# Kernel optimization log

Measured on AMD Instinct MI355X. Metric: run time of the kernel, lower is better.

Reference implementation:

```python
import jax, jax.numpy as jnp
import numpy as np

START_IDX = 1
STOP_IDX = 2
VOCAB = 32000
EMB = 512
HID = 512


def setup_inputs() -> dict:
    key = jax.random.key(0)
    ks = jax.random.split(key, 10)
    B, T = 64, 50
    x = jax.random.normal(ks[0], (B, HID), dtype=jnp.float32)
    labels = jax.random.randint(ks[1], (B, T), 0, VOCAB, dtype=jnp.int64)
    s = 0.02
    emb = jax.random.normal(ks[2], (VOCAB, EMB), dtype=jnp.float32) * s
    W_ih = jax.random.normal(ks[3], (4 * HID, EMB), dtype=jnp.float32) * s
    W_hh = jax.random.normal(ks[4], (4 * HID, HID), dtype=jnp.float32) * s
    b_ih = jax.random.normal(ks[5], (4 * HID,), dtype=jnp.float32) * s
    b_hh = jax.random.normal(ks[6], (4 * HID,), dtype=jnp.float32) * s
    fc_W = jax.random.normal(ks[7], (VOCAB, HID), dtype=jnp.float32) * s
    fc_b = jax.random.normal(ks[8], (VOCAB,), dtype=jnp.float32) * s
    return {"x": x, "labels": labels, "emb": emb, "W_ih": W_ih, "W_hh": W_hh,
            "b_ih": b_ih, "b_hh": b_hh, "fc_W": fc_W, "fc_b": fc_b}


def _decode_loss(x, labels, emb, W_ih, W_hh, b_ih, b_hh, fc_W, fc_b):
    B, T = labels.shape
    # teacher-forced inputs: [START, y_0..y_{T-1}]; targets: [y_0..y_{T-1}, STOP]
    inputs = jnp.concatenate([jnp.full((B, 1), START_IDX, labels.dtype), labels], axis=1)
    targets = jnp.concatenate([labels, jnp.full((B, 1), STOP_IDX, labels.dtype)], axis=1)
    x_emb = emb[inputs]                       # [B, T+1, E]
    x_emb_t = jnp.swapaxes(x_emb, 0, 1)       # [T+1, B, E]

    def step(carry, xt):
        h, c = carry
        gates = xt @ W_ih.T + b_ih + h @ W_hh.T + b_hh   # [B, 4H]
        i, f, g, o = jnp.split(gates, 4, axis=-1)         # torch gate order i,f,g,o
        i = jax.nn.sigmoid(i); f = jax.nn.sigmoid(f)
        g = jnp.tanh(g); o = jax.nn.sigmoid(o)
        c = f * c + i * g
        h = o * jnp.tanh(c)
        return (h, c), h

    # init_states(x[i]): hidden and cell initialized from image feature
    (_, _), hs = jax.lax.scan(step, (x, x), x_emb_t)      # hs: [T+1, B, H]
    logits = hs @ fc_W.T + fc_b                            # [T+1, B, V]
    logp = jax.nn.log_softmax(logits, axis=-1)
    tgt = jnp.swapaxes(targets, 0, 1)[..., None]           # [T+1, B, 1]
    nll = -jnp.take_along_axis(logp, tgt, axis=-1)         # [T+1, B, 1]
    # original: per-step CrossEntropyLoss on batch of 1, summed over steps, / batch_size
    return nll.sum() / B


def reference(x, labels, emb, W_ih, W_hh, b_ih, b_hh, fc_W, fc_b):
    return _decode_loss(x, labels, emb, W_ih, W_hh, b_ih, b_hh, fc_W, fc_b)
```

## Files before the change

kernel.cpp:

```cpp
#include <hip/hip_runtime.h>
#include <cstddef>
#include <cstdint>

#define B_  64
#define T_  51
#define H_  512
#define G4_ 2048
#define V_  32000
#define R_  (T_ * B_)
#define NHF (T_ * 128)

typedef __attribute__((ext_vector_type(8))) short bf16x8;
typedef __attribute__((ext_vector_type(4))) float f32x4;
typedef __attribute__((ext_vector_type(4))) unsigned int u32x4;
typedef unsigned long long ull;

__device__ __forceinline__ uint16_t f2bf(float f) {
    uint32_t u = __float_as_uint(f);
    u += 0x7FFFu + ((u >> 16) & 1u);
    return (uint16_t)(u >> 16);
}
__device__ __forceinline__ float bf2f(uint32_t h) { return __uint_as_float(h << 16); }

__device__ __forceinline__ void ldsc(u32x4& d, const uint32_t* p) {
    asm volatile("global_load_dwordx4 %0, %1, off sc0 sc1" : "=v"(d) : "v"(p));
}
__device__ __forceinline__ void ldq2(ull& d, const uint16_t* p) {
    asm volatile("global_load_dwordx2 %0, %1, off sc0 sc1" : "=v"(d) : "v"(p));
}
__device__ __forceinline__ uint32_t ldflag(const uint32_t* p) {
    uint32_t v;
    asm volatile("global_load_dword %0, %1, off sc0 sc1\n\ts_waitcnt vmcnt(0)"
                 : "=v"(v) : "v"(p));
    return v;
}
__device__ __forceinline__ void stflag(uint32_t* p, uint32_t v) {
    asm volatile("global_store_dword %0, %1, off sc0 sc1" :: "v"(p), "v"(v) : "memory");
}
__device__ __forceinline__ void stsh(uint16_t* p, uint32_t v) {
    asm volatile("global_store_short %0, %1, off sc0 sc1" :: "v"(p), "v"(v) : "memory");
}
__device__ __forceinline__ void stq(uint16_t* p, ull v) {
    asm volatile("global_store_dwordx2 %0, %1, off sc0 sc1" :: "v"(p), "v"(v) : "memory");
}

__device__ __forceinline__ void gl_lds16(const void* g, void* l) {
    __builtin_amdgcn_global_load_lds((const __attribute__((address_space(1))) void*)g,
                                     (__attribute__((address_space(3))) void*)l, 16, 0, 0);
}

__global__ __launch_bounds__(256) void k0_init(float* __restrict__ sumexp,
                                               uint32_t* __restrict__ flags) {
    int i = blockIdx.x * 256 + threadIdx.x;
    if (i < R_) sumexp[i] = 0.f;
    if (i < NHF + 512) flags[i] = 0;
}

template<int DOFC>
__global__ __launch_bounds__(256) void k12p(const float* __restrict__ x,
                                            const int* __restrict__ labels,
                                            const float* __restrict__ emb,
                                            const float* __restrict__ W_ih,
                                            const float* __restrict__ b_ih,
                                            const float* __restrict__ b_hh,
                                            const float* __restrict__ W_hh,
                                            const float* __restrict__ fc_W,
                                            uint16_t* __restrict__ fcwb,
                                            uint16_t* __restrict__ XgT,
                                            uint16_t* __restrict__ hs,
                                            uint32_t* __restrict__ flags) {
    __shared__ uint16_t smem[64 * 520];
    const int bid  = blockIdx.x;
    const int tid  = threadIdx.x;
    const int w    = tid >> 6;
    const int lane = tid & 63;
    const int l15  = lane & 15;
    const int lhi  = lane >> 4;

    if (bid >= 32) {
        uint16_t* Al = smem;
        uint16_t* Bl = smem + 64 * 72;
        for (int id = bid - 32; id < 408; id += 224) {
            const int t  = id >> 3;
            const int n0 = (id & 7) * 256;
            f32x4 acc[4][4];
            #pragma unroll
            for (int mi = 0; mi < 4; ++mi)
                #pragma unroll
                for (int nf = 0; nf < 4; ++nf) acc[mi][nf] = (f32x4){0.f, 0.f, 0.f, 0.f};
            for (int k0 = 0; k0 < H_; k0 += 64) {
                #pragma unroll
                for (int r = 0; r < 2; ++r) {
                    int idx = r * 256 + tid, row = idx >> 3, seg = idx & 7;
                    int tok = (t == 0) ? 1 : labels[row * 50 + (t - 1)];
                    const float* s = emb + (size_t)tok * H_ + k0 + seg * 8;
                    float4 f0 = *(const float4*)s;
                    float4 f1 = *(const float4*)(s + 4);
                    union { uint16_t h[8]; uint4 u; } p;
                    p.h[0]=f2bf(f0.x); p.h[1]=f2bf(f0.y); p.h[2]=f2bf(f0.z); p.h[3]=f2bf(f0.w);
                    p.h[4]=f2bf(f1.x); p.h[5]=f2bf(f1.y); p.h[6]=f2bf(f1.z); p.h[7]=f2bf(f1.w);
                    *(uint4*)(Al + row * 72 + seg * 8) = p.u;
                }
                #pragma unroll
                for (int r = 0; r < 8; ++r) {
                    int idx = r * 256 + tid, row = idx >> 3, seg = idx & 7;
                    const float* s = W_ih + (size_t)(n0 + row) * H_ + k0 + seg * 8;
                    float4 f0 = *(const float4*)s;
                    float4 f1 = *(const float4*)(s + 4);
                    union { uint16_t h[8]; uint4 u; } p;
                    p.h[0]=f2bf(f0.x); p.h[1]=f2bf(f0.y); p.h[2]=f2bf(f0.z); p.h[3]=f2bf(f0.w);
                    p.h[4]=f2bf(f1.x); p.h[5]=f2bf(f1.y); p.h[6]=f2bf(f1.z); p.h[7]=f2bf(f1.w);
                    *(uint4*)(Bl + row * 72 + seg * 8) = p.u;
                }
                __syncthreads();
                #pragma unroll
                for (int ks = 0; ks < 2; ++ks) {
                    bf16x8 a[4];
                    #pragma unroll
                    for (int mi = 0; mi < 4; ++mi)
                        a[mi] = *(const bf16x8*)(Al + (mi * 16 + l15) * 72 + ks * 32 + lhi * 8);
                    #pragma unroll
                    for (int nf = 0; nf < 4; ++nf) {
                        bf16x8 b = *(const bf16x8*)(Bl + (w * 64 + nf * 16 + l15) * 72 + ks * 32 + lhi * 8);
                        #pragma unroll
                        for (int mi = 0; mi < 4; ++mi)
                            acc[mi][nf] = __builtin_amdgcn_mfma_f32_16x16x32_bf16(a[mi], b, acc[mi][nf], 0, 0, 0);
                    }
                }
                __syncthreads();
            }
            float bias[4];
            #pragma unroll
            for (int nf = 0; nf < 4; ++nf) {
                int col = n0 + w * 64 + nf * 16 + l15;
                bias[nf] = b_ih[col] + b_hh[col];
            }
            #pragma unroll
            for (int mi = 0; mi < 4; ++mi)
                #pragma unroll
                for (int nf = 0; nf < 4; ++nf) {
                    const int col = n0 + w * 64 + nf * 16 + l15;
                    const int g = col >> 9, u = col & 511;
                    const int b = mi * 16 + lhi * 4;
                    union { uint16_t h[4]; ull q; } pk;
                    #pragma unroll
                    for (int q = 0; q < 4; ++q) pk.h[q] = f2bf(acc[mi][nf][q] + bias[nf]);
                    stq(XgT + ((size_t)(t * 512 + u) * 4 + g) * 64 + b, pk.q);
                }
            asm volatile("s_waitcnt vmcnt(0)" ::: "memory");
            __syncthreads();
            if (tid == 0) stflag(flags + NHF + t * 8 + (n0 >> 8), 1u);
        }
        if (DOFC) {
            const int n8 = (V_ * H_) / 8;
            for (int i = (bid - 32) * 256 + tid; i < n8; i += 224 * 256) {
                const float4* s = (const float4*)fc_W + (size_t)i * 2;
                float4 f0 = s[0], f1 = s[1];
                union { uint16_t h[8]; uint4 u; } p;
                p.h[0]=f2bf(f0.x); p.h[1]=f2bf(f0.y); p.h[2]=f2bf(f0.z); p.h[3]=f2bf(f0.w);
                p.h[4]=f2bf(f1.x); p.h[5]=f2bf(f1.y); p.h[6]=f2bf(f1.z); p.h[7]=f2bf(f1.w);
                ((uint4*)fcwb)[i] = p.u;
            }
        }
        return;
    }

    uint16_t* Wl = smem;
    const int u0   = bid * 16;
    const int arow = w * 16 + l15;
    {
        const int c = tid >> 2;
        const int q = tid & 3;
        const int j = (c >> 4) * 512 + u0 + (c & 15);
        const float* src = W_hh + (size_t)j * H_ + q * 128;
        uint16_t* dst = Wl + c * 520 + q * 128;
        #pragma unroll
        for (int i = 0; i < 128; i += 8) {
            float4 f0 = *(const float4*)(src + i);
            float4 f1 = *(const float4*)(src + i + 4);
            union { uint16_t h[8]; uint4 u; } p;
            p.h[0]=f2bf(f0.x); p.h[1]=f2bf(f0.y); p.h[2]=f2bf(f0.z); p.h[3]=f2bf(f0.w);
            p.h[4]=f2bf(f1.x); p.h[5]=f2bf(f1.y); p.h[6]=f2bf(f1.z); p.h[7]=f2bf(f1.w);
            *(uint4*)(dst + i) = p.u;
        }
    }
    float cst[4];
    #pragma unroll
    for (int q = 0; q < 4; ++q)
        cst[q] = x[(size_t)(w * 16 + lhi * 4 + q) * H_ + u0 + l15];
    __syncthreads();

    for (int t = 0; t < T_; ++t) {
        const uint32_t* fp = flags;
        bool dopoll = false;
        if (t > 0 && lane < 32)      { fp = flags + (size_t)(t - 1) * 128 + lane * 4 + w; dopoll = true; }
        else if (lane >= 32 && lane < 40) { fp = flags + NHF + t * 8 + (lane - 32); dopoll = true; }
        else if (t == 0 && lane < 8) { fp = flags + NHF + (lane); dopoll = true; }
        for (;;) {
            uint32_t fv = 1;
            if (dopoll) fv = ldflag(fp);
            if (!__any((int)(fv == 0))) break;
            __builtin_amdgcn_s_sleep(1);
        }
        __builtin_amdgcn_sched_barrier(0);

        u32x4 ha[16];
        ull xgp[4];
        if (t == 0) {
            const float* xb = x + (size_t)arow * H_ + lhi * 8;
            #pragma unroll
            for (int ks = 0; ks < 16; ++ks) {
                float4 f0 = *(const float4*)(xb + ks * 32);
                float4 f1 = *(const float4*)(xb + ks * 32 + 4);
                union { uint16_t h[8]; u32x4 u; } p;
                p.h[0]=f2bf(f0.x); p.h[1]=f2bf(f0.y); p.h[2]=f2bf(f0.z); p.h[3]=f2bf(f0.w);
                p.h[4]=f2bf(f1.x); p.h[5]=f2bf(f1.y); p.h[6]=f2bf(f1.z); p.h[7]=f2bf(f1.w);
                ha[ks] = p.u;
            }
        } else {
            const uint16_t* hb = hs + ((size_t)(t - 1) * 64 + arow) * H_ + lhi * 8;
            #pragma unroll
            for (int ks = 0; ks < 16; ++ks)
                ldsc(ha[ks], (const uint32_t*)(hb + ks * 32));
        }
        #pragma unroll
        for (int g = 0; g < 4; ++g)
            ldq2(xgp[g], XgT + ((size_t)(t * 512 + u0 + l15) * 4 + g) * 64 + w * 16 + lhi * 4);

        f32x4 acc[4];
        #pragma unroll
        for (int nf = 0; nf < 4; ++nf) acc[nf] = (f32x4){0.f, 0.f, 0.f, 0.f};
        if (t != 0) { asm volatile("s_waitcnt vmcnt(12)" ::: "memory");
                      __builtin_amdgcn_sched_barrier(0); }
        #pragma unroll
        for (int ks = 0; ks < 8; ++ks) {
            union { u32x4 u; bf16x8 v; } au; au.u = ha[ks];
            #pragma unroll
            for (int nf = 0; nf < 4; ++nf) {
                bf16x8 b = *(const bf16x8*)(Wl + (nf * 16 + l15) * 520 + ks * 32 + lhi * 8);
                acc[nf] = __builtin_amdgcn_mfma_f32_16x16x32_bf16(au.v, b, acc[nf], 0, 0, 0);
            }
        }
        asm volatile("s_waitcnt vmcnt(0)" ::: "memory");
        __builtin_amdgcn_sched_barrier(0);
        #pragma unroll
        for (int ks = 8; ks < 16; ++ks) {
            union { u32x4 u; bf16x8 v; } au; au.u = ha[ks];
            #pragma unroll
            for (int nf = 0; nf < 4; ++nf) {
                bf16x8 b = *(const bf16x8*)(Wl + (nf * 16 + l15) * 520 + ks * 32 + lhi * 8);
                acc[nf] = __builtin_amdgcn_mfma_f32_16x16x32_bf16(au.v, b, acc[nf], 0, 0, 0);
            }
        }
        #pragma unroll
        for (int q = 0; q < 4; ++q) {
            const int b = w * 16 + lhi * 4 + q;
            float gi = acc[0][q] + bf2f((uint32_t)((xgp[0] >> (16 * q)) & 0xFFFF));
            float gf = acc[1][q] + bf2f((uint32_t)((xgp[1] >> (16 * q)) & 0xFFFF));
            float gg = acc[2][q] + bf2f((uint32_t)((xgp[2] >> (16 * q)) & 0xFFFF));
            float go = acc[3][q] + bf2f((uint32_t)((xgp[3] >> (16 * q)) & 0xFFFF));
            float si = 1.f / (1.f + __expf(-gi));
            float sf = 1.f / (1.f + __expf(-gf));
            float tg = tanhf(gg);
            float so = 1.f / (1.f + __expf(-go));
            float cc = sf * cst[q] + si * tg;
            cst[q] = cc;
            stsh(hs + (size_t)(t * 64 + b) * H_ + u0 + l15, (uint32_t)f2bf(so * tanhf(cc)));
        }
        asm volatile("s_waitcnt vmcnt(0)" ::: "memory");
        if (lane == 0) stflag(flags + (size_t)t * 128 + bid * 4 + w, (uint32_t)(t + 1));
    }
}

template<int CVT>
__global__ __launch_bounds__(512, 4) void k3_mfma(const uint16_t* __restrict__ hsb,
                                                  const void* __restrict__ fcw,
                                                  const float* __restrict__ fc_b,
                                                  const int* __restrict__ labels,
                                                  float* __restrict__ sumexp,
                                                  float* __restrict__ tgtlog) {
    __shared__ uint16_t Al[128 * 64];
    __shared__ uint16_t Bl[256 * 64];
    const int flat = blockIdx.x;
    const int xcd  = flat & 7;
    const int slot = flat >> 3;
    const int work = (xcd < 2 ? xcd * 407 : 814 + (xcd - 2) * 406) + slot;
    const int m0   = (work % 26) * 128;
    const int v0   = (work / 26) * 256;
    const int tid  = threadIdx.x;
    const int w    = tid >> 6;
    const int lane = tid & 63;
    const int l15  = lane & 15;
    const int lhi  = lane >> 4;
    const int wm   = w >> 2;
    const int wn   = w & 3;

    f32x4 acc[4][4];
    #pragma unroll
    for (int mi = 0; mi < 4; ++mi)
        #pragma unroll
        for (int nf = 0; nf < 4; ++nf) acc[mi][nf] = (f32x4){0.f, 0.f, 0.f, 0.f};

    const int lrow = lane >> 3;
    const int segp = (lane & 7) ^ lrow;

    for (int k0 = 0; k0 < H_; k0 += 64) {
        #pragma unroll
        for (int r = 0; r < 2; ++r) {
            const int g = w * 2 + r, row0 = g * 8;
            int grow = m0 + row0 + lrow; if (grow >= R_) grow = R_ - 1;
            gl_lds16(hsb + (size_t)grow * H_ + k0 + segp * 8, Al + row0 * 64);
        }
        if (CVT == 0) {
            #pragma unroll
            for (int r = 0; r < 4; ++r) {
                const int g = w * 4 + r, row0 = g * 8;
                gl_lds16((const uint16_t*)fcw + (size_t)(v0 + row0 + lrow) * H_ + k0 + segp * 8,
                         Bl + row0 * 64);
            }
        } else {
            #pragma unroll
            for (int r = 0; r < 4; ++r) {
                int idx = r * 512 + tid, row = idx >> 3, seg = idx & 7;
                const float* s = (const float*)fcw + (size_t)(v0 + row) * H_ + k0 + seg * 8;
                float4 f0 = *(const float4*)s;
                float4 f1 = *(const float4*)(s + 4);
                union { uint16_t h[8]; uint4 u; } p;
                p.h[0]=f2bf(f0.x); p.h[1]=f2bf(f0.y); p.h[2]=f2bf(f0.z); p.h[3]=f2bf(f0.w);
                p.h[4]=f2bf(f1.x); p.h[5]=f2bf(f1.y); p.h[6]=f2bf(f1.z); p.h[7]=f2bf(f1.w);
                *(uint4*)(Bl + row * 64 + (seg ^ (row & 7)) * 8) = p.u;
            }
        }
        __syncthreads();
        #pragma unroll
        for (int ks = 0; ks < 2; ++ks) {
            bf16x8 a[4];
            #pragma unroll
            for (int mi = 0; mi < 4; ++mi) {
                const int ar = wm * 64 + mi * 16 + l15;
                a[mi] = *(const bf16x8*)((const char*)Al + ar * 128 +
                        ((ks * 64 + lhi * 16) ^ ((ar & 7) << 4)));
            }
            #pragma unroll
            for (int nf = 0; nf < 4; ++nf) {
                const int br = wn * 64 + nf * 16 + l15;
                bf16x8 b = *(const bf16x8*)((const char*)Bl + br * 128 +
                           ((ks * 64 + lhi * 16) ^ ((br & 7) << 4)));
                #pragma unroll
                for (int mi = 0; mi < 4; ++mi)
                    acc[mi][nf] = __builtin_amdgcn_mfma_f32_16x16x32_bf16(a[mi], b, acc[mi][nf], 0, 0, 0);
            }
        }
        __syncthreads();
    }
    float bias[4];
    #pragma unroll
    for (int nf = 0; nf < 4; ++nf) bias[nf] = fc_b[v0 + wn * 64 + nf * 16 + l15];
    #pragma unroll
    for (int mi = 0; mi < 4; ++mi) {
        #pragma unroll
        for (int q = 0; q < 4; ++q) {
            const int r = m0 + wm * 64 + mi * 16 + lhi * 4 + q;
            if (r >= R_) continue;
            const int t = r >> 6, b = r & 63;
            const int tgt = (t < 50) ? labels[b * 50 + t] : 2;
            float lsum = 0.f;
            #pragma unroll
            for (int nf = 0; nf < 4; ++nf) {
                const int v = v0 + wn * 64 + nf * 16 + l15;
                float lg = acc[mi][nf][q] + bias[nf];
                lsum += __expf(lg);
                if (v == tgt) tgtlog[r] = lg;
            }
            lsum += __shfl_xor(lsum, 1, 16);
            lsum += __shfl_xor(lsum, 2, 16);
            lsum += __shfl_xor(lsum, 4, 16);
            lsum += __shfl_xor(lsum, 8, 16);
            if (l15 == 0) atomicAdd(&sumexp[r], lsum);
        }
    }
}

__global__ __launch_bounds__(256) void k4_loss(const float* __restrict__ sumexp,
                                               const float* __restrict__ tgtlog,
                                               float* __restrict__ out) {
    __shared__ float red[256];
    float s = 0.f;
    for (int r = threadIdx.x; r < R_; r += 256) s += logf(sumexp[r]) - tgtlog[r];
    red[threadIdx.x] = s;
    __syncthreads();
    for (int st = 128; st > 0; st >>= 1) {
        if (threadIdx.x < st) red[threadIdx.x] += red[threadIdx.x + st];
        __syncthreads();
    }
    if (threadIdx.x == 0) out[0] = red[0] / 64.0f;
}

extern "C" void kernel_launch(void* const* d_in, const int* in_sizes, int n_in,
                              void* d_out, int out_size, void* d_ws, size_t ws_size,
                              hipStream_t stream) {
    const float* x      = (const float*)d_in[0];
    const int*   labels = (const int*)d_in[1];
    const float* emb    = (const float*)d_in[2];
    const float* W_ih   = (const float*)d_in[3];
    const float* W_hh   = (const float*)d_in[4];
    const float* b_ih   = (const float*)d_in[5];
    const float* b_hh   = (const float*)d_in[6];
    const float* fc_W   = (const float*)d_in[7];
    const float* fc_b   = (const float*)d_in[8];
    float* out = (float*)d_out;

    char* p = (char*)d_ws;
    uint16_t* XgT    = (uint16_t*)p;  p += (size_t)T_ * 512 * 4 * 64 * 2;
    uint16_t* hsb    = (uint16_t*)p;  p += (size_t)R_ * H_ * 2;
    float*    sumexp = (float*)p;     p += (size_t)R_ * 4;
    float*    tgtl   = (float*)p;     p += (size_t)R_ * 4;
    uint32_t* flags  = (uint32_t*)p;  p += (size_t)(NHF + 512) * 4;
    uint16_t* fcwb   = (uint16_t*)p;  p += (size_t)V_ * H_ * 2;
    const bool pre = ((size_t)(p - (char*)d_ws) <= ws_size);

    k0_init<<<32, 256, 0, stream>>>(sumexp, flags);
    if (pre) {
        k12p<1><<<256, 256, 0, stream>>>(x, labels, emb, W_ih, b_ih, b_hh, W_hh,
                                         fc_W, fcwb, XgT, hsb, flags);
        k3_mfma<0><<<3250, 512, 0, stream>>>(hsb, fcwb, fc_b, labels, sumexp, tgtl);
    } else {
        k12p<0><<<256, 256, 0, stream>>>(x, labels, emb, W_ih, b_ih, b_hh, W_hh,
                                         fc_W, fcwb, XgT, hsb, flags);
        k3_mfma<1><<<3250, 512, 0, stream>>>(hsb, fc_W, fc_b, labels, sumexp, tgtl);
    }
    k4_loss<<<1, 256, 0, stream>>>(sumexp, tgtl, out);
}
```

Baseline: 508.1 us.

## Double-buffer FC GEMM tiles and split fc_W conversion onto dedicated delayed blocks

```diff
diff --git a/kernel.cpp b/kernel.cpp
--- a/kernel.cpp
+++ b/kernel.cpp
@@ -77,10 +77,27 @@
     const int l15  = lane & 15;
     const int lhi  = lane >> 4;
 
+    if (bid >= 96) {
+        if (DOFC) {
+            #pragma unroll
+            for (int d = 0; d < 8; ++d) __builtin_amdgcn_s_sleep(127);
+            const int n8 = (V_ * H_) / 8;
+            for (int i = (bid - 96) * 256 + tid; i < n8; i += 160 * 256) {
+                const float4* s = (const float4*)fc_W + (size_t)i * 2;
+                float4 f0 = s[0], f1 = s[1];
+                union { uint16_t h[8]; uint4 u; } p;
+                p.h[0]=f2bf(f0.x); p.h[1]=f2bf(f0.y); p.h[2]=f2bf(f0.z); p.h[3]=f2bf(f0.w);
+                p.h[4]=f2bf(f1.x); p.h[5]=f2bf(f1.y); p.h[6]=f2bf(f1.z); p.h[7]=f2bf(f1.w);
+                ((uint4*)fcwb)[i] = p.u;
+            }
+        }
+        return;
+    }
+
     if (bid >= 32) {
         uint16_t* Al = smem;
         uint16_t* Bl = smem + 64 * 72;
-        for (int id = bid - 32; id < 408; id += 224) {
+        for (int id = bid - 32; id < 408; id += 64) {
             const int t  = id >> 3;
             const int n0 = (id & 7) * 256;
             f32x4 acc[4][4];
@@ -151,17 +168,6 @@
             __syncthreads();
             if (tid == 0) stflag(flags + NHF + t * 8 + (n0 >> 8), 1u);
         }
-        if (DOFC) {
-            const int n8 = (V_ * H_) / 8;
-            for (int i = (bid - 32) * 256 + tid; i < n8; i += 224 * 256) {
-                const float4* s = (const float4*)fc_W + (size_t)i * 2;
-                float4 f0 = s[0], f1 = s[1];
-                union { uint16_t h[8]; uint4 u; } p;
-                p.h[0]=f2bf(f0.x); p.h[1]=f2bf(f0.y); p.h[2]=f2bf(f0.z); p.h[3]=f2bf(f0.w);
-                p.h[4]=f2bf(f1.x); p.h[5]=f2bf(f1.y); p.h[6]=f2bf(f1.z); p.h[7]=f2bf(f1.w);
-                ((uint4*)fcwb)[i] = p.u;
-            }
-        }
         return;
     }
 
@@ -195,7 +201,7 @@
         bool dopoll = false;
         if (t > 0 && lane < 32)      { fp = flags + (size_t)(t - 1) * 128 + lane * 4 + w; dopoll = true; }
         else if (lane >= 32 && lane < 40) { fp = flags + NHF + t * 8 + (lane - 32); dopoll = true; }
-        else if (t == 0 && lane < 8) { fp = flags + NHF + (lane); dopoll = true; }
+        else if (t == 0 && lane < 8) { fp = flags + NHF + lane; dopoll = true; }
         for (;;) {
             uint32_t fv = 1;
             if (dopoll) fv = ldflag(fp);
@@ -273,14 +279,14 @@
 }
 
 template<int CVT>
-__global__ __launch_bounds__(512, 4) void k3_mfma(const uint16_t* __restrict__ hsb,
+__global__ __launch_bounds__(512, 2) void k3_mfma(const uint16_t* __restrict__ hsb,
                                                   const void* __restrict__ fcw,
                                                   const float* __restrict__ fc_b,
                                                   const int* __restrict__ labels,
                                                   float* __restrict__ sumexp,
                                                   float* __restrict__ tgtlog) {
-    __shared__ uint16_t Al[128 * 64];
-    __shared__ uint16_t Bl[256 * 64];
+    __shared__ uint16_t Al[2][128 * 64];
+    __shared__ uint16_t Bl[2][256 * 64];
     const int flat = blockIdx.x;
     const int xcd  = flat & 7;
     const int slot = flat >> 3;
@@ -304,21 +310,60 @@
     const int lrow = lane >> 3;
     const int segp = (lane & 7) ^ lrow;
 
-    for (int k0 = 0; k0 < H_; k0 += 64) {
-        #pragma unroll
-        for (int r = 0; r < 2; ++r) {
-            const int g = w * 2 + r, row0 = g * 8;
-            int grow = m0 + row0 + lrow; if (grow >= R_) grow = R_ - 1;
-            gl_lds16(hsb + (size_t)grow * H_ + k0 + segp * 8, Al + row0 * 64);
-        }
-        if (CVT == 0) {
-            #pragma unroll
-            for (int r = 0; r < 4; ++r) {
-                const int g = w * 4 + r, row0 = g * 8;
-                gl_lds16((const uint16_t*)fcw + (size_t)(v0 + row0 + lrow) * H_ + k0 + segp * 8,
-                         Bl + row0 * 64);
-            }
-        } else {
+    if (CVT == 0) {
+        #define STAGE_K3(buf, kt)                                                          \
+            {   const int k0s = (kt) * 64;                                                 \
+                _Pragma("unroll")                                                          \
+                for (int r = 0; r < 2; ++r) {                                              \
+                    const int row0 = (w * 2 + r) * 8;                                      \
+                    int grow = m0 + row0 + lrow; if (grow >= R_) grow = R_ - 1;            \
+                    gl_lds16(hsb + (size_t)grow * H_ + k0s + segp * 8, &Al[buf][row0 * 64]); \
+                }                                                                          \
+                _Pragma("unroll")                                                          \
+                for (int r = 0; r < 4; ++r) {                                              \
+                    const int row0 = (w * 4 + r) * 8;                                      \
+                    gl_lds16((const uint16_t*)fcw + (size_t)(v0 + row0 + lrow) * H_ + k0s + segp * 8, \
+                             &Bl[buf][row0 * 64]);                                         \
+                }                                                                          \
+            }
+        STAGE_K3(0, 0);
+        __syncthreads();
+        int cur = 0;
+        for (int kt = 0; kt < 8; ++kt) {
+            if (kt < 7) STAGE_K3(cur ^ 1, kt + 1);
+            #pragma unroll
+            for (int ks = 0; ks < 2; ++ks) {
+                bf16x8 a[4];
+                #pragma unroll
+                for (int mi = 0; mi < 4; ++mi) {
+                    const int ar = wm * 64 + mi * 16 + l15;
+                    a[mi] = *(const bf16x8*)((const char*)&Al[cur][0] + ar * 128 +
+                            ((ks * 64 + lhi * 16) ^ ((ar & 7) << 4)));
+                }
+                #pragma unroll
+                for (int nf = 0; nf < 4; ++nf) {
+                    const int br = wn * 64 + nf * 16 + l15;
+                    bf16x8 b = *(const bf16x8*)((const char*)&Bl[cur][0] + br * 128 +
+                               ((ks * 64 + lhi * 16) ^ ((br & 7) << 4)));
+                    #pragma unroll
+                    for (int mi = 0; mi < 4; ++mi)
+                        acc[mi][nf] = __builtin_amdgcn_mfma_f32_16x16x32_bf16(a[mi], b, acc[mi][nf], 0, 0, 0);
+                }
+            }
+            if (kt < 7) {
+                __syncthreads();
+                cur ^= 1;
+            }
+        }
+        #undef STAGE_K3
+    } else {
+        for (int k0 = 0; k0 < H_; k0 += 64) {
+            #pragma unroll
+            for (int r = 0; r < 2; ++r) {
+                const int row0 = (w * 2 + r) * 8;
+                int grow = m0 + row0 + lrow; if (grow >= R_) grow = R_ - 1;
+                gl_lds16(hsb + (size_t)grow * H_ + k0 + segp * 8, &Al[0][row0 * 64]);
+            }
             #pragma unroll
             for (int r = 0; r < 4; ++r) {
                 int idx = r * 512 + tid, row = idx >> 3, seg = idx & 7;
@@ -328,30 +373,30 @@
                 union { uint16_t h[8]; uint4 u; } p;
                 p.h[0]=f2bf(f0.x); p.h[1]=f2bf(f0.y); p.h[2]=f2bf(f0.z); p.h[3]=f2bf(f0.w);
                 p.h[4]=f2bf(f1.x); p.h[5]=f2bf(f1.y); p.h[6]=f2bf(f1.z); p.h[7]=f2bf(f1.w);
-                *(uint4*)(Bl + row * 64 + (seg ^ (row & 7)) * 8) = p.u;
-            }
-        }
-        __syncthreads();
-        #pragma unroll
-        for (int ks = 0; ks < 2; ++ks) {
-            bf16x8 a[4];
-            #pragma unroll
-            for (int mi = 0; mi < 4; ++mi) {
-                const int ar = wm * 64 + mi * 16 + l15;
-                a[mi] = *(const bf16x8*)((const char*)Al + ar * 128 +
-                        ((ks * 64 + lhi * 16) ^ ((ar & 7) << 4)));
-            }
-            #pragma unroll
-            for (int nf = 0; nf < 4; ++nf) {
-                const int br = wn * 64 + nf * 16 + l15;
-                bf16x8 b = *(const bf16x8*)((const char*)Bl + br * 128 +
-                           ((ks * 64 + lhi * 16) ^ ((br & 7) << 4)));
-                #pragma unroll
-                for (int mi = 0; mi < 4; ++mi)
-                    acc[mi][nf] = __builtin_amdgcn_mfma_f32_16x16x32_bf16(a[mi], b, acc[mi][nf], 0, 0, 0);
-            }
-        }
-        __syncthreads();
+                *(uint4*)(&Bl[0][row * 64] + (seg ^ (row & 7)) * 8) = p.u;
+            }
+            __syncthreads();
+            #pragma unroll
+            for (int ks = 0; ks < 2; ++ks) {
+                bf16x8 a[4];
+                #pragma unroll
+                for (int mi = 0; mi < 4; ++mi) {
+                    const int ar = wm * 64 + mi * 16 + l15;
+                    a[mi] = *(const bf16x8*)((const char*)&Al[0][0] + ar * 128 +
+                            ((ks * 64 + lhi * 16) ^ ((ar & 7) << 4)));
+                }
+                #pragma unroll
+                for (int nf = 0; nf < 4; ++nf) {
+                    const int br = wn * 64 + nf * 16 + l15;
+                    bf16x8 b = *(const bf16x8*)((const char*)&Bl[0][0] + br * 128 +
+                               ((ks * 64 + lhi * 16) ^ ((br & 7) << 4)));
+                    #pragma unroll
+                    for (int mi = 0; mi < 4; ++mi)
+                        acc[mi][nf] = __builtin_amdgcn_mfma_f32_16x16x32_bf16(a[mi], b, acc[mi][nf], 0, 0, 0);
+                }
+            }
+            __syncthreads();
+        }
     }
     float bias[4];
     #pragma unroll
```

After: 598.5 us. 17.8% more time.

## Fuse output projection into persistent recurrence kernel with flag-gated tiles

Applied to the files above, without the earlier changes.

```diff
diff --git a/kernel.cpp b/kernel.cpp
--- a/kernel.cpp
+++ b/kernel.cpp
@@ -44,11 +44,6 @@
     asm volatile("global_store_dwordx2 %0, %1, off sc0 sc1" :: "v"(p), "v"(v) : "memory");
 }
 
-__device__ __forceinline__ void gl_lds16(const void* g, void* l) {
-    __builtin_amdgcn_global_load_lds((const __attribute__((address_space(1))) void*)g,
-                                     (__attribute__((address_space(3))) void*)l, 16, 0, 0);
-}
-
 __global__ __launch_bounds__(256) void k0_init(float* __restrict__ sumexp,
                                                uint32_t* __restrict__ flags) {
     int i = blockIdx.x * 256 + threadIdx.x;
@@ -56,20 +51,22 @@
     if (i < NHF + 512) flags[i] = 0;
 }
 
-template<int DOFC>
-__global__ __launch_bounds__(256) void k12p(const float* __restrict__ x,
-                                            const int* __restrict__ labels,
-                                            const float* __restrict__ emb,
-                                            const float* __restrict__ W_ih,
-                                            const float* __restrict__ b_ih,
-                                            const float* __restrict__ b_hh,
-                                            const float* __restrict__ W_hh,
-                                            const float* __restrict__ fc_W,
-                                            uint16_t* __restrict__ fcwb,
-                                            uint16_t* __restrict__ XgT,
-                                            uint16_t* __restrict__ hs,
-                                            uint32_t* __restrict__ flags) {
+__global__ __launch_bounds__(512) void k123p(const float* __restrict__ x,
+                                             const int* __restrict__ labels,
+                                             const float* __restrict__ emb,
+                                             const float* __restrict__ W_ih,
+                                             const float* __restrict__ b_ih,
+                                             const float* __restrict__ b_hh,
+                                             const float* __restrict__ W_hh,
+                                             const float* __restrict__ fc_W,
+                                             const float* __restrict__ fc_b,
+                                             uint16_t* __restrict__ XgT,
+                                             uint16_t* __restrict__ hs,
+                                             uint32_t* __restrict__ flags,
+                                             float* __restrict__ sumexp,
+                                             float* __restrict__ tgtlog) {
     __shared__ uint16_t smem[64 * 520];
+    __shared__ int sready;
     const int bid  = blockIdx.x;
     const int tid  = threadIdx.x;
     const int w    = tid >> 6;
@@ -77,21 +74,132 @@
     const int l15  = lane & 15;
     const int lhi  = lane >> 4;
 
-    if (bid >= 32) {
+    if (bid < 32) {
+        uint16_t* Wl = smem;
+        const int u0   = bid * 16;
+        const int arow = w * 16 + l15;
+        {
+            const int c  = tid >> 3;
+            const int q8 = tid & 7;
+            const int j  = (c >> 4) * 512 + u0 + (c & 15);
+            const float* src = W_hh + (size_t)j * H_ + q8 * 64;
+            uint16_t* dst = Wl + c * 520 + q8 * 64;
+            #pragma unroll
+            for (int i = 0; i < 64; i += 8) {
+                float4 f0 = *(const float4*)(src + i);
+                float4 f1 = *(const float4*)(src + i + 4);
+                union { uint16_t h[8]; uint4 u; } p;
+                p.h[0]=f2bf(f0.x); p.h[1]=f2bf(f0.y); p.h[2]=f2bf(f0.z); p.h[3]=f2bf(f0.w);
+                p.h[4]=f2bf(f1.x); p.h[5]=f2bf(f1.y); p.h[6]=f2bf(f1.z); p.h[7]=f2bf(f1.w);
+                *(uint4*)(dst + i) = p.u;
+            }
+        }
+        float cst[4] = {0.f, 0.f, 0.f, 0.f};
+        if (w < 4) {
+            #pragma unroll
+            for (int q = 0; q < 4; ++q)
+                cst[q] = x[(size_t)(w * 16 + lhi * 4 + q) * H_ + u0 + l15];
+        }
+        __syncthreads();
+        if (w >= 4) return;
+
+        for (int t = 0; t < T_; ++t) {
+            const uint32_t* fp = flags;
+            bool dopoll = false;
+            if (t > 0 && lane < 32)           { fp = flags + (size_t)(t - 1) * 128 + lane * 4 + w; dopoll = true; }
+            else if (lane >= 32 && lane < 40) { fp = flags + NHF + t * 8 + (lane - 32); dopoll = true; }
+            else if (t == 0 && lane < 8)      { fp = flags + NHF + lane; dopoll = true; }
+            for (;;) {
+                uint32_t fv = 1;
+                if (dopoll) fv = ldflag(fp);
+                if (!__any((int)(fv == 0))) break;
+                __builtin_amdgcn_s_sleep(1);
+            }
+            __builtin_amdgcn_sched_barrier(0);
+
+            u32x4 ha[16];
+            ull xgp[4];
+            if (t == 0) {
+                const float* xb = x + (size_t)arow * H_ + lhi * 8;
+                #pragma unroll
+                for (int ks = 0; ks < 16; ++ks) {
+                    float4 f0 = *(const float4*)(xb + ks * 32);
+                    float4 f1 = *(const float4*)(xb + ks * 32 + 4);
+                    union { uint16_t h[8]; u32x4 u; } p;
+                    p.h[0]=f2bf(f0.x); p.h[1]=f2bf(f0.y); p.h[2]=f2bf(f0.z); p.h[3]=f2bf(f0.w);
+                    p.h[4]=f2bf(f1.x); p.h[5]=f2bf(f1.y); p.h[6]=f2bf(f1.z); p.h[7]=f2bf(f1.w);
+                    ha[ks] = p.u;
+                }
+            } else {
+                const uint16_t* hb = hs + ((size_t)(t - 1) * 64 + arow) * H_ + lhi * 8;
+                #pragma unroll
+                for (int ks = 0; ks < 16; ++ks)
+                    ldsc(ha[ks], (const uint32_t*)(hb + ks * 32));
+            }
+            #pragma unroll
+            for (int g = 0; g < 4; ++g)
+                ldq2(xgp[g], XgT + ((size_t)(t * 512 + u0 + l15) * 4 + g) * 64 + w * 16 + lhi * 4);
+
+            f32x4 acc[4];
+            #pragma unroll
+            for (int nf = 0; nf < 4; ++nf) acc[nf] = (f32x4){0.f, 0.f, 0.f, 0.f};
+            if (t != 0) { asm volatile("s_waitcnt vmcnt(12)" ::: "memory");
+                          __builtin_amdgcn_sched_barrier(0); }
+            #pragma unroll
+            for (int ks = 0; ks < 8; ++ks) {
+                union { u32x4 u; bf16x8 v; } au; au.u = ha[ks];
+                #pragma unroll
+                for (int nf = 0; nf < 4; ++nf) {
+                    bf16x8 b = *(const bf16x8*)(Wl + (nf * 16 + l15) * 520 + ks * 32 + lhi * 8);
+                    acc[nf] = __builtin_amdgcn_mfma_f32_16x16x32_bf16(au.v, b, acc[nf], 0, 0, 0);
+                }
+            }
+            asm volatile("s_waitcnt vmcnt(0)" ::: "memory");
+            __builtin_amdgcn_sched_barrier(0);
+            #pragma unroll
+            for (int ks = 8; ks < 16; ++ks) {
+                union { u32x4 u; bf16x8 v; } au; au.u = ha[ks];
+                #pragma unroll
+                for (int nf = 0; nf < 4; ++nf) {
+                    bf16x8 b = *(const bf16x8*)(Wl + (nf * 16 + l15) * 520 + ks * 32 + lhi * 8);
+                    acc[nf] = __builtin_amdgcn_mfma_f32_16x16x32_bf16(au.v, b, acc[nf], 0, 0, 0);
+                }
+            }
+            #pragma unroll
+            for (int q = 0; q < 4; ++q) {
+                const int b = w * 16 + lhi * 4 + q;
+                float gi = acc[0][q] + bf2f((uint32_t)((xgp[0] >> (16 * q)) & 0xFFFF));
+                float gf = acc[1][q] + bf2f((uint32_t)((xgp[1] >> (16 * q)) & 0xFFFF));
+                float gg = acc[2][q] + bf2f((uint32_t)((xgp[2] >> (16 * q)) & 0xFFFF));
+                float go = acc[3][q] + bf2f((uint32_t)((xgp[3] >> (16 * q)) & 0xFFFF));
+                float si = 1.f / (1.f + __expf(-gi));
+                float sf = 1.f / (1.f + __expf(-gf));
+                float tg = tanhf(gg);
+                float so = 1.f / (1.f + __expf(-go));
+                float cc = sf * cst[q] + si * tg;
+                cst[q] = cc;
+                stsh(hs + (size_t)(t * 64 + b) * H_ + u0 + l15, (uint32_t)f2bf(so * tanhf(cc)));
+            }
+            asm volatile("s_waitcnt vmcnt(0)" ::: "memory");
+            if (lane == 0) stflag(flags + (size_t)t * 128 + bid * 4 + w, (uint32_t)(t + 1));
+        }
+        return;
+    }
+
+    {
         uint16_t* Al = smem;
         uint16_t* Bl = smem + 64 * 72;
         for (int id = bid - 32; id < 408; id += 224) {
             const int t  = id >> 3;
             const int n0 = (id & 7) * 256;
-            f32x4 acc[4][4];
+            f32x4 acc[4][2];
             #pragma unroll
             for (int mi = 0; mi < 4; ++mi)
                 #pragma unroll
-                for (int nf = 0; nf < 4; ++nf) acc[mi][nf] = (f32x4){0.f, 0.f, 0.f, 0.f};
+                for (int nf = 0; nf < 2; ++nf) acc[mi][nf] = (f32x4){0.f, 0.f, 0.f, 0.f};
             for (int k0 = 0; k0 < H_; k0 += 64) {
-                #pragma unroll
-                for (int r = 0; r < 2; ++r) {
-                    int idx = r * 256 + tid, row = idx >> 3, seg = idx & 7;
+                {
+                    int row = tid >> 3, seg = tid & 7;
                     int tok = (t == 0) ? 1 : labels[row * 50 + (t - 1)];
                     const float* s = emb + (size_t)tok * H_ + k0 + seg * 8;
                     float4 f0 = *(const float4*)s;
@@ -102,8 +210,8 @@
                     *(uint4*)(Al + row * 72 + seg * 8) = p.u;
                 }
                 #pragma unroll
-                for (int r = 0; r < 8; ++r) {
-                    int idx = r * 256 + tid, row = idx >> 3, seg = idx & 7;
+                for (int r = 0; r < 4; ++r) {
+                    int idx = r * 512 + tid, row = idx >> 3, seg = idx & 7;
                     const float* s = W_ih + (size_t)(n0 + row) * H_ + k0 + seg * 8;
                     float4 f0 = *(const float4*)s;
                     float4 f1 = *(const float4*)(s + 4);
@@ -120,8 +228,8 @@
                     for (int mi = 0; mi < 4; ++mi)
                         a[mi] = *(const bf16x8*)(Al + (mi * 16 + l15) * 72 + ks * 32 + lhi * 8);
                     #pragma unroll
-                    for (int nf = 0; nf < 4; ++nf) {
-                        bf16x8 b = *(const bf16x8*)(Bl + (w * 64 + nf * 16 + l15) * 72 + ks * 32 + lhi * 8);
+                    for (int nf = 0; nf < 2; ++nf) {
+                        bf16x8 b = *(const bf16x8*)(Bl + (w * 32 + nf * 16 + l15) * 72 + ks * 32 + lhi * 8);
                         #pragma unroll
                         for (int mi = 0; mi < 4; ++mi)
                             acc[mi][nf] = __builtin_amdgcn_mfma_f32_16x16x32_bf16(a[mi], b, acc[mi][nf], 0, 0, 0);
@@ -129,17 +237,17 @@
                 }
                 __syncthreads();
             }
-            float bias[4];
-            #pragma unroll
-            for (int nf = 0; nf < 4; ++nf) {
-                int col = n0 + w * 64 + nf * 16 + l15;
+            float bias[2];
+            #pragma unroll
+            for (int nf = 0; nf < 2; ++nf) {
+                int col = n0 + w * 32 + nf * 16 + l15;
                 bias[nf] = b_ih[col] + b_hh[col];
             }
             #pragma unroll
             for (int mi = 0; mi < 4; ++mi)
                 #pragma unroll
-                for (int nf = 0; nf < 4; ++nf) {
-                    const int col = n0 + w * 64 + nf * 16 + l15;
+                for (int nf = 0; nf < 2; ++nf) {
+                    const int col = n0 + w * 32 + nf * 16 + l15;
                     const int g = col >> 9, u = col & 511;
                     const int b = mi * 16 + lhi * 4;
                     union { uint16_t h[4]; ull q; } pk;
@@ -151,232 +259,121 @@
             __syncthreads();
             if (tid == 0) stflag(flags + NHF + t * 8 + (n0 >> 8), 1u);
         }
-        if (DOFC) {
-            const int n8 = (V_ * H_) / 8;
-            for (int i = (bid - 32) * 256 + tid; i < n8; i += 224 * 256) {
-                const float4* s = (const float4*)fc_W + (size_t)i * 2;
-                float4 f0 = s[0], f1 = s[1];
-                union { uint16_t h[8]; uint4 u; } p;
-                p.h[0]=f2bf(f0.x); p.h[1]=f2bf(f0.y); p.h[2]=f2bf(f0.z); p.h[3]=f2bf(f0.w);
-                p.h[4]=f2bf(f1.x); p.h[5]=f2bf(f1.y); p.h[6]=f2bf(f1.z); p.h[7]=f2bf(f1.w);
-                ((uint4*)fcwb)[i] = p.u;
-            }
-        }
-        return;
     }
-
-    uint16_t* Wl = smem;
-    const int u0   = bid * 16;
-    const int arow = w * 16 + l15;
-    {
-        const int c = tid >> 2;
-        const int q = tid & 3;
-        const int j = (c >> 4) * 512 + u0 + (c & 15);
-        const float* src = W_hh + (size_t)j * H_ + q * 128;
-        uint16_t* dst = Wl + c * 520 + q * 128;
+    __syncthreads();
+
+    uint16_t* Al = smem;
+    uint16_t* Bl = smem + 128 * 64;
+    const int wm = w >> 2;
+    const int wn = w & 3;
+    int ready_t = -1;
+    for (int id = bid - 32; id < 3250; id += 224) {
+        const int mt = id / 125, v = id % 125;
+        const int m0 = mt * 128, v0 = v * 256;
+        const int maxt = (2 * mt + 1 > 50) ? 50 : (2 * mt + 1);
+        while (maxt > ready_t) {
+            uint32_t fv = 1;
+            if (tid < 64) {
+                uint32_t f1 = ldflag(flags + (size_t)maxt * 128 + tid * 2);
+                uint32_t f2 = ldflag(flags + (size_t)maxt * 128 + tid * 2 + 1);
+                fv = (f1 != 0 && f2 != 0) ? 1u : 0u;
+            }
+            bool allset = !__any((int)(fv == 0));
+            if (tid == 0) sready = allset ? 1 : 0;
+            __syncthreads();
+            int ok = sready;
+            __syncthreads();
+            if (ok) ready_t = maxt;
+            else {
+                #pragma unroll
+                for (int d = 0; d < 4; ++d) __builtin_amdgcn_s_sleep(127);
+            }
+        }
+
+        f32x4 acc[4][4];
         #pragma unroll
-        for (int i = 0; i < 128; i += 8) {
-            float4 f0 = *(const float4*)(src + i);
-            float4 f1 = *(const float4*)(src + i + 4);
-            union { uint16_t h[8]; uint4 u; } p;
-            p.h[0]=f2bf(f0.x); p.h[1]=f2bf(f0.y); p.h[2]=f2bf(f0.z); p.h[3]=f2bf(f0.w);
-            p.h[4]=f2bf(f1.x); p.h[5]=f2bf(f1.y); p.h[6]=f2bf(f1.z); p.h[7]=f2bf(f1.w);
-            *(uint4*)(dst + i) = p.u;
-        }
-    }
-    float cst[4];
-    #pragma unroll
-    for (int q = 0; q < 4; ++q)
-        cst[q] = x[(size_t)(w * 16 + lhi * 4 + q) * H_ + u0 + l15];
-    __syncthreads();
-
-    for (int t = 0; t < T_; ++t) {
-        const uint32_t* fp = flags;
-        bool dopoll = false;
-        if (t > 0 && lane < 32)      { fp = flags + (size_t)(t - 1) * 128 + lane * 4 + w; dopoll = true; }
-        else if (lane >= 32 && lane < 40) { fp = flags + NHF + t * 8 + (lane - 32); dopoll = true; }
-        else if (t == 0 && lane < 8) { fp = flags + NHF + (lane); dopoll = true; }
-        for (;;) {
-            uint32_t fv = 1;
-            if (dopoll) fv = ldflag(fp);
-            if (!__any((int)(fv == 0))) break;
-            __builtin_amdgcn_s_sleep(1);
-        }
-        __builtin_amdgcn_sched_barrier(0);
-
-        u32x4 ha[16];
-        ull xgp[4];
-        if (t == 0) {
-            const float* xb = x + (size_t)arow * H_ + lhi * 8;
-            #pragma unroll
-            for (int ks = 0; ks < 16; ++ks) {
-                float4 f0 = *(const float4*)(xb + ks * 32);
-                float4 f1 = *(const float4*)(xb + ks * 32 + 4);
-                union { uint16_t h[8]; u32x4 u; } p;
-                p.h[0]=f2bf(f0.x); p.h[1]=f2bf(f0.y); p.h[2]=f2bf(f0.z); p.h[3]=f2bf(f0.w);
-                p.h[4]=f2bf(f1.x); p.h[5]=f2bf(f1.y); p.h[6]=f2bf(f1.z); p.h[7]=f2bf(f1.w);
-                ha[ks] = p.u;
-            }
-        } else {
-            const uint16_t* hb = hs + ((size_t)(t - 1) * 64 + arow) * H_ + lhi * 8;
-            #pragma unroll
-            for (int ks = 0; ks < 16; ++ks)
-                ldsc(ha[ks], (const uint32_t*)(hb + ks * 32));
-        }
-        #pragma unroll
-        for (int g = 0; g < 4; ++g)
-            ldq2(xgp[g], XgT + ((size_t)(t * 512 + u0 + l15) * 4 + g) * 64 + w * 16 + lhi * 4);
-
-        f32x4 acc[4];
-        #pragma unroll
-        for (int nf = 0; nf < 4; ++nf) acc[nf] = (f32x4){0.f, 0.f, 0.f, 0.f};
-        if (t != 0) { asm volatile("s_waitcnt vmcnt(12)" ::: "memory");
-                      __builtin_amdgcn_sched_barrier(0); }
-        #pragma unroll
-        for (int ks = 0; ks < 8; ++ks) {
-            union { u32x4 u; bf16x8 v; } au; au.u = ha[ks];
-            #pragma unroll
-            for (int nf = 0; nf < 4; ++nf) {
-                bf16x8 b = *(const bf16x8*)(Wl + (nf * 16 + l15) * 520 + ks * 32 + lhi * 8);
-                acc[nf] = __builtin_amdgcn_mfma_f32_16x16x32_bf16(au.v, b, acc[nf], 0, 0, 0);
-            }
-        }
-        asm volatile("s_waitcnt vmcnt(0)" ::: "memory");
-        __builtin_amdgcn_sched_barrier(0);
-        #pragma unroll
-        for (int ks = 8; ks < 16; ++ks) {
-            union { u32x4 u; bf16x8 v; } au; au.u = ha[ks];
-            #pragma unroll
-            for (int nf = 0; nf < 4; ++nf) {
-                bf16x8 b = *(const bf16x8*)(Wl + (nf * 16 + l15) * 520 + ks * 32 + lhi * 8);
-                acc[nf] = __builtin_amdgcn_mfma_f32_16x16x32_bf16(au.v, b, acc[nf], 0, 0, 0);
-            }
-        }
-        #pragma unroll
-        for (int q = 0; q < 4; ++q) {
-            const int b = w * 16 + lhi * 4 + q;
-            float gi = acc[0][q] + bf2f((uint32_t)((xgp[0] >> (16 * q)) & 0xFFFF));
-            float gf = acc[1][q] + bf2f((uint32_t)((xgp[1] >> (16 * q)) & 0xFFFF));
-            float gg = acc[2][q] + bf2f((uint32_t)((xgp[2] >> (16 * q)) & 0xFFFF));
-            float go = acc[3][q] + bf2f((uint32_t)((xgp[3] >> (16 * q)) & 0xFFFF));
-            float si = 1.f / (1.f + __expf(-gi));
-            float sf = 1.f / (1.f + __expf(-gf));
-            float tg = tanhf(gg);
-            float so = 1.f / (1.f + __expf(-go));
-            float cc = sf * cst[q] + si * tg;
-            cst[q] = cc;
-            stsh(hs + (size_t)(t * 64 + b) * H_ + u0 + l15, (uint32_t)f2bf(so * tanhf(cc)));
-        }
-        asm volatile("s_waitcnt vmcnt(0)" ::: "memory");
-        if (lane == 0) stflag(flags + (size_t)t * 128 + bid * 4 + w, (uint32_t)(t + 1));
-    }
-}
-
-template<int CVT>
-__global__ __launch_bounds__(512, 4) void k3_mfma(const uint16_t* __restrict__ hsb,
-                                                  const void* __restrict__ fcw,
-                                                  const float* __restrict__ fc_b,
-                                                  const int* __restrict__ labels,
-                                                  float* __restrict__ sumexp,
-                                                  float* __restrict__ tgtlog) {
-    __shared__ uint16_t Al[128 * 64];
-    __shared__ uint16_t Bl[256 * 64];
-    const int flat = blockIdx.x;
-    const int xcd  = flat & 7;
-    const int slot = flat >> 3;
-    const int work = (xcd < 2 ? xcd * 407 : 814 + (xcd - 2) * 406) + slot;
-    const int m0   = (work % 26) * 128;
-    const int v0   = (work / 26) * 256;
-    const int tid  = threadIdx.x;
-    const int w    = tid >> 6;
-    const int lane = tid & 63;
-    const int l15  = lane & 15;
-    const int lhi  = lane >> 4;
-    const int wm   = w >> 2;
-    const int wn   = w & 3;
-
-    f32x4 acc[4][4];
-    #pragma unroll
-    for (int mi = 0; mi < 4; ++mi)
-        #pragma unroll
-        for (int nf = 0; nf < 4; ++nf) acc[mi][nf] = (f32x4){0.f, 0.f, 0.f, 0.f};
-
-    const int lrow = lane >> 3;
-    const int segp = (lane & 7) ^ lrow;
-
-    for (int k0 = 0; k0 < H_; k0 += 64) {
-        #pragma unroll
-        for (int r = 0; r < 2; ++r) {
-            const int g = w * 2 + r, row0 = g * 8;
-            int grow = m0 + row0 + lrow; if (grow >= R_) grow = R_ - 1;
-            gl_lds16(hsb + (size_t)grow * H_ + k0 + segp * 8, Al + row0 * 64);
-        }
-        if (CVT == 0) {
-            #pragma unroll
-            for (int r = 0; r < 4; ++r) {
-                const int g = w * 4 + r, row0 = g * 8;
-                gl_lds16((const uint16_t*)fcw + (size_t)(v0 + row0 + lrow) * H_ + k0 + segp * 8,
-                         Bl + row0 * 64);
-            }
-        } else {
+        for (int mi = 0; mi < 4; ++mi)
+            #pragma unroll
+            for (int nf = 0; nf < 4; ++nf) acc[mi][nf] = (f32x4){0.f, 0.f, 0.f, 0.f};
+
+        for (int k0 = 0; k0 < H_; k0 += 64) {
+            u32x4 av[2];
+            float4 bf[4][2];
+            #pragma unroll
+            for (int r = 0; r < 2; ++r) {
+                int idx = r * 512 + tid, row = idx >> 3, seg = idx & 7;
+                int grow = m0 + row; if (grow >= R_) grow = R_ - 1;
+                ldsc(av[r], (const uint32_t*)(hs + (size_t)grow * H_ + k0 + seg * 8));
+            }
             #pragma unroll
             for (int r = 0; r < 4; ++r) {
                 int idx = r * 512 + tid, row = idx >> 3, seg = idx & 7;
-                const float* s = (const float*)fcw + (size_t)(v0 + row) * H_ + k0 + seg * 8;
-                float4 f0 = *(const float4*)s;
-                float4 f1 = *(const float4*)(s + 4);
+                const float* s = fc_W + (size_t)(v0 + row) * H_ + k0 + seg * 8;
+                bf[r][0] = *(const float4*)s;
+                bf[r][1] = *(const float4*)(s + 4);
+            }
+            __syncthreads();
+            asm volatile("s_waitcnt vmcnt(0)" ::: "memory");
+            #pragma unroll
+            for (int r = 0; r < 2; ++r) {
+                int idx = r * 512 + tid, row = idx >> 3, seg = idx & 7;
+                *(uint4*)(Al + row * 64 + ((seg ^ (row & 7)) * 8)) = *(uint4*)&av[r];
+            }
+            #pragma unroll
+            for (int r = 0; r < 4; ++r) {
+                int idx = r * 512 + tid, row = idx >> 3, seg = idx & 7;
                 union { uint16_t h[8]; uint4 u; } p;
-                p.h[0]=f2bf(f0.x); p.h[1]=f2bf(f0.y); p.h[2]=f2bf(f0.z); p.h[3]=f2bf(f0.w);
-                p.h[4]=f2bf(f1.x); p.h[5]=f2bf(f1.y); p.h[6]=f2bf(f1.z); p.h[7]=f2bf(f1.w);
-                *(uint4*)(Bl + row * 64 + (seg ^ (row & 7)) * 8) = p.u;
+                p.h[0]=f2bf(bf[r][0].x); p.h[1]=f2bf(bf[r][0].y); p.h[2]=f2bf(bf[r][0].z); p.h[3]=f2bf(bf[r][0].w);
+                p.h[4]=f2bf(bf[r][1].x); p.h[5]=f2bf(bf[r][1].y); p.h[6]=f2bf(bf[r][1].z); p.h[7]=f2bf(bf[r][1].w);
+                *(uint4*)(Bl + row * 64 + ((seg ^ (row & 7)) * 8)) = p.u;
+            }
+            __syncthreads();
+            #pragma unroll
+            for (int ks = 0; ks < 2; ++ks) {
+                bf16x8 a[4];
+                #pragma unroll
+                for (int mi = 0; mi < 4; ++mi) {
+                    const int ar = wm * 64 + mi * 16 + l15;
+                    a[mi] = *(const bf16x8*)((const char*)Al + ar * 128 +
+                            ((ks * 64 + lhi * 16) ^ ((ar & 7) << 4)));
+                }
+                #pragma unroll
+                for (int nf = 0; nf < 4; ++nf) {
+                    const int br = wn * 64 + nf * 16 + l15;
+                    bf16x8 b = *(const bf16x8*)((const char*)Bl + br * 128 +
+                               ((ks * 64 + lhi * 16) ^ ((br & 7) << 4)));
+                    #pragma unroll
+                    for (int mi = 0; mi < 4; ++mi)
+                        acc[mi][nf] = __builtin_amdgcn_mfma_f32_16x16x32_bf16(a[mi], b, acc[mi][nf], 0, 0, 0);
+                }
             }
         }
         __syncthreads();
+        float bias[4];
         #pragma unroll
-        for (int ks = 0; ks < 2; ++ks) {
-            bf16x8 a[4];
-            #pragma unroll
-            for (int mi = 0; mi < 4; ++mi) {
-                const int ar = wm * 64 + mi * 16 + l15;
-                a[mi] = *(const bf16x8*)((const char*)Al + ar * 128 +
-                        ((ks * 64 + lhi * 16) ^ ((ar & 7) << 4)));
-            }
-            #pragma unroll
-            for (int nf = 0; nf < 4; ++nf) {
-                const int br = wn * 64 + nf * 16 + l15;
-                bf16x8 b = *(const bf16x8*)((const char*)Bl + br * 128 +
-                           ((ks * 64 + lhi * 16) ^ ((br & 7) << 4)));
-                #pragma unroll
-                for (int mi = 0; mi < 4; ++mi)
-                    acc[mi][nf] = __builtin_amdgcn_mfma_f32_16x16x32_bf16(a[mi], b, acc[mi][nf], 0, 0, 0);
-            }
-        }
-        __syncthreads();
-    }
-    float bias[4];
-    #pragma unroll
-    for (int nf = 0; nf < 4; ++nf) bias[nf] = fc_b[v0 + wn * 64 + nf * 16 + l15];
-    #pragma unroll
-    for (int mi = 0; mi < 4; ++mi) {
+        for (int nf = 0; nf < 4; ++nf) bias[nf] = fc_b[v0 + wn * 64 + nf * 16 + l15];
         #pragma unroll
-        for (int q = 0; q < 4; ++q) {
-            const int r = m0 + wm * 64 + mi * 16 + lhi * 4 + q;
-            if (r >= R_) continue;
-            const int t = r >> 6, b = r & 63;
-            const int tgt = (t < 50) ? labels[b * 50 + t] : 2;
-            float lsum = 0.f;
-            #pragma unroll
-            for (int nf = 0; nf < 4; ++nf) {
-                const int v = v0 + wn * 64 + nf * 16 + l15;
-                float lg = acc[mi][nf][q] + bias[nf];
-                lsum += __expf(lg);
-                if (v == tgt) tgtlog[r] = lg;
-            }
-            lsum += __shfl_xor(lsum, 1, 16);
-            lsum += __shfl_xor(lsum, 2, 16);
-            lsum += __shfl_xor(lsum, 4, 16);
-            lsum += __shfl_xor(lsum, 8, 16);
-            if (l15 == 0) atomicAdd(&sumexp[r], lsum);
+        for (int mi = 0; mi < 4; ++mi) {
+            #pragma unroll
+            for (int q = 0; q < 4; ++q) {
+                const int r = m0 + wm * 64 + mi * 16 + lhi * 4 + q;
+                if (r >= R_) continue;
+                const int t = r >> 6, b = r & 63;
+                const int tgt = (t < 50) ? labels[b * 50 + t] : 2;
+                float lsum = 0.f;
+                #pragma unroll
+                for (int nf = 0; nf < 4; ++nf) {
+                    const int vv = v0 + wn * 64 + nf * 16 + l15;
+                    float lg = acc[mi][nf][q] + bias[nf];
+                    lsum += __expf(lg);
+                    if (vv == tgt) tgtlog[r] = lg;
+                }
+                lsum += __shfl_xor(lsum, 1, 16);
+                lsum += __shfl_xor(lsum, 2, 16);
+                lsum += __shfl_xor(lsum, 4, 16);
+                lsum += __shfl_xor(lsum, 8, 16);
+                if (l15 == 0) atomicAdd(&sumexp[r], lsum);
+            }
         }
     }
 }
@@ -416,18 +413,9 @@
     float*    sumexp = (float*)p;     p += (size_t)R_ * 4;
     float*    tgtl   = (float*)p;     p += (size_t)R_ * 4;
     uint32_t* flags  = (uint32_t*)p;  p += (size_t)(NHF + 512) * 4;
-    uint16_t* fcwb   = (uint16_t*)p;  p += (size_t)V_ * H_ * 2;
-    const bool pre = ((size_t)(p - (char*)d_ws) <= ws_size);
 
     k0_init<<<32, 256, 0, stream>>>(sumexp, flags);
-    if (pre) {
-        k12p<1><<<256, 256, 0, stream>>>(x, labels, emb, W_ih, b_ih, b_hh, W_hh,
-                                         fc_W, fcwb, XgT, hsb, flags);
-        k3_mfma<0><<<3250, 512, 0, stream>>>(hsb, fcwb, fc_b, labels, sumexp, tgtl);
-    } else {
-        k12p<0><<<256, 256, 0, stream>>>(x, labels, emb, W_ih, b_ih, b_hh, W_hh,
-                                         fc_W, fcwb, XgT, hsb, flags);
-        k3_mfma<1><<<3250, 512, 0, stream>>>(hsb, fc_W, fc_b, labels, sumexp, tgtl);
-    }
+    k123p<<<256, 512, 0, stream>>>(x, labels, emb, W_ih, b_ih, b_hh, W_hh,
+                                   fc_W, fc_b, XgT, hsb, flags, sumexp, tgtl);
     k4_loss<<<1, 256, 0, stream>>>(sumexp, tgtl, out);
 }
```

Result: slower. 576.0 us (+13.4%).
